# Optimization experiments

Measured on AMD Instinct MI355X. Metric: run time of the kernel, lower is better.

The kernel has to match this reference:

```python
import jax, jax.numpy as jnp
import numpy as np

P = 2; NH = 16; HS = 1024; NL = 12; NC = 1000
B, D, H, W = 32, 64, 32, 32
LFEAT = P * P * D  # 256 per-patch feature dim


def _sincos_1d(dim, pos):
    omega = np.arange(dim // 2, dtype=np.float64) / (dim / 2.0)
    omega = 1.0 / 10000 ** omega
    out = np.einsum('m,d->md', pos.reshape(-1), omega)
    return np.concatenate([np.sin(out), np.cos(out)], axis=1)


def _pos_embed(dim, grid_size):
    g = np.arange(grid_size, dtype=np.float32)
    grid = np.stack(np.meshgrid(g, g), axis=0).reshape(2, 1, grid_size, grid_size)
    emb = np.concatenate([_sincos_1d(dim // 2, grid[0]), _sincos_1d(dim // 2, grid[1])], axis=1)
    return jnp.asarray(emb, dtype=jnp.float32)


def setup_inputs() -> dict:
    key = jax.random.key(0)
    ks = iter(jax.random.split(key, 40))
    def w(shape, s=0.02):
        return jax.random.normal(next(ks), shape, jnp.float32) * s
    return {
        'x': jax.random.normal(next(ks), (B, D, H, W), jnp.float32),
        'y': jax.random.randint(next(ks), (B,), 0, NC),
        't': jax.random.randint(next(ks), (B,), 0, 1000),
        'proj_w': w((LFEAT, HS)), 'proj_b': jnp.zeros((HS,), jnp.float32),
        'pos_embed': _pos_embed(HS, H // P),
        'emb_table': w((NC + 1, HS)),
        'blk_mod_w': w((NL, HS, 6 * HS)), 'blk_mod_b': jnp.zeros((NL, 6 * HS), jnp.float32),
        'blk_wq': w((NL, HS, HS)), 'blk_bq': jnp.zeros((NL, HS), jnp.float32),
        'blk_wk': w((NL, HS, HS)), 'blk_bk': jnp.zeros((NL, HS), jnp.float32),
        'blk_wv': w((NL, HS, HS)), 'blk_bv': jnp.zeros((NL, HS), jnp.float32),
        'blk_wo': w((NL, HS, HS)), 'blk_bo': jnp.zeros((NL, HS), jnp.float32),
        'blk_fc1_w': w((NL, HS, 4 * HS)), 'blk_fc1_b': jnp.zeros((NL, 4 * HS), jnp.float32),
        'blk_fc2_w': w((NL, 4 * HS, HS)), 'blk_fc2_b': jnp.zeros((NL, HS), jnp.float32),
        'fin_mod_w': w((HS, 2 * HS)), 'fin_mod_b': jnp.zeros((2 * HS,), jnp.float32),
        'fin_out_w': w((HS, LFEAT)), 'fin_out_b': jnp.zeros((LFEAT,), jnp.float32),
    }


def _ln(z):
    mu = jnp.mean(z, -1, keepdims=True)
    var = jnp.mean((z - mu) ** 2, -1, keepdims=True)
    return (z - mu) * jax.lax.rsqrt(var + 1e-5)


def _forward(x, y, t, proj_w, proj_b, pos_embed, emb_table,
             blk_mod_w, blk_mod_b, blk_wq, blk_bq, blk_wk, blk_bk, blk_wv, blk_bv,
             blk_wo, blk_bo, blk_fc1_w, blk_fc1_b, blk_fc2_w, blk_fc2_b,
             fin_mod_w, fin_mod_b, fin_out_w, fin_out_b):
    Bc, Dc, Hc, Wc = x.shape
    Hp, Wp = Hc // P, Wc // P
    dh = HS // NH
    # patchify_flatten: (B, L, P*P*D)
    tok = x.reshape(Bc, Dc, Hp, P, Wp, P).transpose(0, 2, 4, 3, 5, 1).reshape(Bc, Hp * Wp, P * P * Dc)
    tok = tok @ proj_w + proj_b + pos_embed[None]
    # timestep_embedding: [cos, sin] order per source
    half = HS // 2
    freqs = jnp.exp(-jnp.log(jnp.float32(10000.0)) * jnp.arange(half, dtype=jnp.float32) / half)
    ang = t.astype(jnp.float32)[:, None] * freqs[None]
    c = jnp.concatenate([jnp.cos(ang), jnp.sin(ang)], axis=-1) + emb_table[y]
    c_act = jax.nn.silu(c)  # each block applies silu to c (c is not mutated across blocks)

    def block(xc, p):
        mw, mb, wq, bq, wk, bk, wv, bv, wo, bo, f1w, f1b, f2w, f2b = p
        mod = c_act @ mw + mb
        sh_a, sc_a, g_a, sh_m, sc_m, g_m = jnp.split(mod, 6, axis=1)
        hx = _ln(xc) * (1 + sc_a[:, None]) + sh_a[:, None]
        def heads(z, wz, bz):
            return (z @ wz + bz).reshape(Bc, -1, NH, dh).transpose(0, 2, 1, 3)
        q, k, v = heads(hx, wq, bq), heads(hx, wk, bk), heads(hx, wv, bv)
        logits = jnp.einsum('bhqd,bhkd->bhqk', q, k) / jnp.sqrt(jnp.float32(dh))
        # non-AR mask buffer is all zeros -> no-op
        attn = jax.nn.softmax(logits, axis=-1)
        o = jnp.einsum('bhqk,bhkd->bhqd', attn, v).transpose(0, 2, 1, 3).reshape(Bc, -1, HS)
        xc = xc + g_a[:, None] * (o @ wo + bo)
        hx = _ln(xc) * (1 + sc_m[:, None]) + sh_m[:, None]
        mlp = jax.nn.gelu(hx @ f1w + f1b, approximate=False) @ f2w + f2b
        return xc + g_m[:, None] * mlp, None

    tok, _ = jax.lax.scan(block, tok, (blk_mod_w, blk_mod_b, blk_wq, blk_bq, blk_wk, blk_bk,
                                       blk_wv, blk_bv, blk_wo, blk_bo,
                                       blk_fc1_w, blk_fc1_b, blk_fc2_w, blk_fc2_b))
    fmod = c_act @ fin_mod_w + fin_mod_b
    sh, sc = jnp.split(fmod, 2, axis=1)
    out = (_ln(tok) * (1 + sc[:, None]) + sh[:, None]) @ fin_out_w + fin_out_b
    # unpatchify -> (B, D, H, W)
    return out.reshape(Bc, Hp, Wp, P, P, Dc).transpose(0, 5, 1, 3, 2, 4).reshape(Bc, Dc, Hc, Wc)


def reference(x, y, t, proj_w, proj_b, pos_embed, emb_table,
              blk_mod_w, blk_mod_b, blk_wq, blk_bq, blk_wk, blk_bk, blk_wv, blk_bv,
              blk_wo, blk_bo, blk_fc1_w, blk_fc1_b, blk_fc2_w, blk_fc2_b,
              fin_mod_w, fin_mod_b, fin_out_w, fin_out_b):
    return _forward(x, y, t, proj_w, proj_b, pos_embed, emb_table,
                    blk_mod_w, blk_mod_b, blk_wq, blk_bq, blk_wk, blk_bk, blk_wv, blk_bv,
                    blk_wo, blk_bo, blk_fc1_w, blk_fc1_b, blk_fc2_w, blk_fc2_b,
                    fin_mod_w, fin_mod_b, fin_out_w, fin_out_b)
```

## Files before the change

kernel.cpp:

```cpp
#include <hip/hip_runtime.h>
#include <hip/hip_bf16.h>
#include <math.h>

typedef short s16x8 __attribute__((ext_vector_type(8)));
typedef float f32x4 __attribute__((ext_vector_type(4)));
typedef unsigned short u16;

#define BAR() __builtin_amdgcn_s_barrier()
#define PRIO1() __builtin_amdgcn_s_setprio(1)
#define PRIO0() __builtin_amdgcn_s_setprio(0)
#define VMCNT0() asm volatile("s_waitcnt vmcnt(0)" ::: "memory")

__device__ __forceinline__ u16 f2b(float f) {
    unsigned u = __builtin_bit_cast(unsigned, f);
    u += 0x7fffu + ((u >> 16) & 1u);
    return (u16)(u >> 16);
}
__device__ __forceinline__ f32x4 mfma16(s16x8 a, s16x8 b, f32x4 c) {
    return __builtin_amdgcn_mfma_f32_16x16x32_bf16(a, b, c, 0, 0, 0);
}
__device__ __forceinline__ void gload16(const void* g, void* l) {
    __builtin_amdgcn_global_load_lds((const __attribute__((address_space(1))) unsigned*)g,
                                     (__attribute__((address_space(3))) unsigned*)l, 16, 0, 0);
}

__global__ __launch_bounds__(256) void patchify_kernel(const float* __restrict__ x, u16* __restrict__ out) {
    int idx = blockIdx.x * 256 + threadIdx.x;
    int row = idx >> 8, col = idx & 255;
    int b = row >> 8, ll = row & 255, hp = ll >> 4, wp = ll & 15;
    int pp = col >> 6, d = col & 63;
    out[idx] = f2b(x[(size_t)((b * 64 + d) * 32 + hp * 2 + (pp >> 1)) * 32 + wp * 2 + (pp & 1)]);
}

__global__ __launch_bounds__(256) void cact_kernel(const int* __restrict__ t, const int* __restrict__ y,
                                                   const float* __restrict__ emb, float* __restrict__ cactF) {
    int b = blockIdx.x, tid = threadIdx.x;
    float tv = (float)t[b];
    int yb = y[b];
#pragma unroll
    for (int j = 0; j < 4; ++j) {
        int c = tid * 4 + j;
        int f = (c < 512) ? c : c - 512;
        float freq = __expf(-9.210340371976184f * (float)f * (1.f / 512.f));
        float ang = tv * freq;
        float v = (c < 512) ? cosf(ang) : sinf(ang);
        v += emb[(size_t)yb * 1024 + c];
        v = v / (1.f + __expf(-v));
        cactF[b * 1024 + c] = v;
    }
}

__global__ __launch_bounds__(256) void bcat_kernel(const float* __restrict__ bq, const float* __restrict__ bk,
                                                   const float* __restrict__ bv, float* __restrict__ out) {
    int lyr = blockIdx.x, j = blockIdx.y, tid = threadIdx.x;
    const float* src = (j == 0) ? bq : ((j == 1) ? bk : bv);
    float4 v = ((const float4*)(src + (size_t)lyr * 1024))[tid];
    ((float4*)(out + (size_t)lyr * 3072 + j * 1024))[tid] = v;
}

__global__ __launch_bounds__(256) void mod32_kernel(const float* __restrict__ cactF, const float* __restrict__ W,
                                                    const float* __restrict__ bias, float* __restrict__ out, int N) {
    __shared__ float cs[32 * 256];
    __shared__ float red[4 * 32 * 64];
    int tid = threadIdx.x, lane = tid & 63, kg = tid >> 6;
    int n = blockIdx.x * 64 + lane;
    float acc[32];
#pragma unroll
    for (int r = 0; r < 32; ++r) acc[r] = 0.f;
    for (int ch = 0; ch < 4; ++ch) {
        __syncthreads();
#pragma unroll
        for (int j = 0; j < 8; ++j) {
            int idx = tid * 4 + j * 1024;
            float4 v = *(const float4*)&cactF[(size_t)(idx >> 8) * 1024 + ch * 256 + (idx & 255)];
            *(float4*)&cs[idx] = v;
        }
        __syncthreads();
        const float* Wp = W + (size_t)(ch * 256 + kg * 64) * N + n;
        for (int kk = 0; kk < 64; kk += 4) {
            float w0 = Wp[(size_t)(kk + 0) * N];
            float w1 = Wp[(size_t)(kk + 1) * N];
            float w2 = Wp[(size_t)(kk + 2) * N];
            float w3 = Wp[(size_t)(kk + 3) * N];
            int kb = kg * 64 + kk;
#pragma unroll
            for (int r = 0; r < 32; ++r) {
                float4 cv = *(const float4*)&cs[r * 256 + kb];
                acc[r] += cv.x * w0 + cv.y * w1 + cv.z * w2 + cv.w * w3;
            }
        }
    }
#pragma unroll
    for (int r = 0; r < 32; ++r) red[(kg * 32 + r) * 64 + lane] = acc[r];
    __syncthreads();
    int r = tid >> 3, j0 = (tid & 7) * 8;
#pragma unroll
    for (int jj = 0; jj < 8; ++jj) {
        int nn = j0 + jj;
        float s = red[(0 * 32 + r) * 64 + nn] + red[(1 * 32 + r) * 64 + nn] +
                  red[(2 * 32 + r) * 64 + nn] + red[(3 * 32 + r) * 64 + nn];
        out[(size_t)r * N + blockIdx.x * 64 + nn] = s + bias[blockIdx.x * 64 + nn];
    }
}

__device__ __forceinline__ void tpose_body(float (*tile)[65], const float* __restrict__ in,
                                           u16* __restrict__ out, int R, int C, int r0, int c0, int tid) {
    int rr = tid >> 4, cc = (tid & 15) * 4;
#pragma unroll
    for (int j = 0; j < 4; ++j) {
        float4 v = *(const float4*)&in[(size_t)(r0 + j * 16 + rr) * C + c0 + cc];
        tile[j * 16 + rr][cc]     = v.x;
        tile[j * 16 + rr][cc + 1] = v.y;
        tile[j * 16 + rr][cc + 2] = v.z;
        tile[j * 16 + rr][cc + 3] = v.w;
    }
    __syncthreads();
    int oc = tid >> 3, r8 = (tid & 7) * 8;
#pragma unroll
    for (int j = 0; j < 2; ++j) {
        int ocl = j * 32 + oc;
        s16x8 vv;
#pragma unroll
        for (int e = 0; e < 8; ++e) vv[e] = (short)f2b(tile[r8 + e][ocl]);
        *(s16x8*)&out[(size_t)(c0 + ocl) * R + r0 + r8] = vv;
    }
}

__global__ __launch_bounds__(256) void transpose_cvt64k(const float* __restrict__ in, u16* __restrict__ out,
                                                        int R, int C) {
    __shared__ float tile[64][65];
    tpose_body(tile, in, out, R, C, blockIdx.y * 64, blockIdx.x * 64, threadIdx.x);
}

__global__ __launch_bounds__(256) void transpose_layer(
    const float* __restrict__ wq, const float* __restrict__ wk,
    const float* __restrict__ wv, const float* __restrict__ wo, const float* __restrict__ f1,
    const float* __restrict__ f2,
    u16* __restrict__ qkvT, u16* __restrict__ woT, u16* __restrict__ f1T, u16* __restrict__ f2T) {
    __shared__ float tile[64][65];
    int bid = blockIdx.x, tid = threadIdx.x;
    const float* src; u16* dst; int R, C, tloc;
    if (bid < 256)       { src = wq; dst = qkvT;               R = 1024; C = 1024; tloc = bid; }
    else if (bid < 512)  { src = wk; dst = qkvT + 1024 * 1024; R = 1024; C = 1024; tloc = bid - 256; }
    else if (bid < 768)  { src = wv; dst = qkvT + 2048 * 1024; R = 1024; C = 1024; tloc = bid - 512; }
    else if (bid < 1024) { src = wo; dst = woT;                R = 1024; C = 1024; tloc = bid - 768; }
    else if (bid < 2048) { src = f1; dst = f1T;                R = 1024; C = 4096; tloc = bid - 1024; }
    else                 { src = f2; dst = f2T;                R = 4096; C = 1024; tloc = bid - 2048; }
    int tx = C >> 6;
    int ty = tloc / tx, txi = tloc - ty * tx;
    tpose_body(tile, src, dst, R, C, ty * 64, txi * 64, tid);
}

__global__ __launch_bounds__(256) void ln_mod_kernel(const float* __restrict__ x, const float* __restrict__ modv,
                                                     int mod_ld, int sh_off, int sc_off, u16* __restrict__ out) {
    int row = blockIdx.x, tid = threadIdx.x, b = row >> 8;
    float4 xv = ((const float4*)(x + (size_t)row * 1024))[tid];
    float s = xv.x + xv.y + xv.z + xv.w;
    float s2 = xv.x * xv.x + xv.y * xv.y + xv.z * xv.z + xv.w * xv.w;
#pragma unroll
    for (int d = 1; d < 64; d <<= 1) { s += __shfl_xor(s, d); s2 += __shfl_xor(s2, d); }
    __shared__ float red[8];
    int w = tid >> 6;
    if ((tid & 63) == 0) { red[w] = s; red[4 + w] = s2; }
    __syncthreads();
    s = red[0] + red[1] + red[2] + red[3];
    s2 = red[4] + red[5] + red[6] + red[7];
    float mu = s * (1.f / 1024.f);
    float rs = rsqrtf(s2 * (1.f / 1024.f) - mu * mu + 1e-5f);
    const float* shp = modv + (size_t)b * mod_ld + sh_off;
    const float* scp = modv + (size_t)b * mod_ld + sc_off;
    float4 sh4 = ((const float4*)shp)[tid];
    float4 sc4 = ((const float4*)scp)[tid];
    u16 o0 = f2b((xv.x - mu) * rs * (1.f + sc4.x) + sh4.x);
    u16 o1 = f2b((xv.y - mu) * rs * (1.f + sc4.y) + sh4.y);
    u16 o2 = f2b((xv.z - mu) * rs * (1.f + sc4.z) + sh4.z);
    u16 o3 = f2b((xv.w - mu) * rs * (1.f + sc4.w) + sh4.w);
    unsigned long long pk = (unsigned long long)o0 | ((unsigned long long)o1 << 16) |
                            ((unsigned long long)o2 << 32) | ((unsigned long long)o3 << 48);
    *(unsigned long long*)&out[(size_t)row * 1024 + tid * 4] = pk;
}

template <int EPI>
__global__ __launch_bounds__(512, 1) void gemm8(
    const u16* __restrict__ A, int lda, const u16* __restrict__ Bt, int ldb,
    int M, int N, int K, const float* __restrict__ bias,
    float* __restrict__ outF, u16* __restrict__ outB, int ldc,
    const float* __restrict__ aux1, const float* __restrict__ aux2, int gateOff) {
    __shared__ u16 As[3][256 * 64];
    __shared__ u16 Bs[3][128 * 64];

    const int tid = threadIdx.x, w = tid >> 6, l = tid & 63;
    const int wm = w >> 1, wn = w & 1;

    const int nbn = N >> 7;
    const int orig = blockIdx.x;
    const int cpx = gridDim.x >> 3;
    const int wg = (orig & 7) * cpx + (orig >> 3);
    const int bm = wg / nbn, bn = wg - bm * nbn;
    const int row0 = bm << 8, col0 = bn << 7;

    const int NT = K >> 6;

    const int srow = tid >> 3, sslot = tid & 7;
    const int ksl = sslot ^ (srow & 7);
    const u16* gA = A + (size_t)(row0 + srow) * lda + ksl * 8;
    const u16* gB = Bt + (size_t)(col0 + srow) * ldb + ksl * 8;
    const int lOff = srow * 64 + sslot * 8;

    const int fr = l & 15, fg = l >> 4;
    const int arow = wm * 64 + fr;
    const int brow = wn * 64 + fr;

    f32x4 acc[4][4];
#pragma unroll
    for (int m = 0; m < 4; ++m)
#pragma unroll
        for (int n = 0; n < 4; ++n) acc[m][n] = (f32x4){0.f, 0.f, 0.f, 0.f};

    {
        u16* a0 = &As[0][lOff];
        u16* b0 = &Bs[0][lOff];
#pragma unroll
        for (int a = 0; a < 4; ++a) gload16(gA + (size_t)a * 64 * lda, a0 + a * 4096);
#pragma unroll
        for (int b = 0; b < 2; ++b) gload16(gB + (size_t)b * 64 * ldb, b0 + b * 4096);
        if (NT > 1) {
            u16* a1 = &As[1][lOff];
#pragma unroll
            for (int a = 0; a < 3; ++a) gload16(gA + (size_t)a * 64 * lda + 64, a1 + a * 4096);
        }
    }
    if (NT > 1) { asm volatile("s_waitcnt vmcnt(3)" ::: "memory"); }
    else        { VMCNT0(); }
    BAR();
    __builtin_amdgcn_sched_barrier(0);

    int q = 0;
    for (int t = 0; t < NT; ++t) {
        const u16* ca = As[q];
        const u16* cb = Bs[q];
        const int q1 = (q == 2) ? 0 : q + 1;
        const int q2 = (q1 == 2) ? 0 : q1 + 1;

        s16x8 af[4][2], bf[4][2];
#pragma unroll
        for (int m = 0; m < 4; ++m) {
            int r = arow + m * 16;
            af[m][0] = *(const s16x8*)(ca + r * 64 + ((fg     ^ (r & 7)) * 8));
            af[m][1] = *(const s16x8*)(ca + r * 64 + (((4 + fg) ^ (r & 7)) * 8));
        }
#pragma unroll
        for (int n = 0; n < 2; ++n) {
            int r = brow + n * 16;
            bf[n][0] = *(const s16x8*)(cb + r * 64 + ((fg     ^ (r & 7)) * 8));
            bf[n][1] = *(const s16x8*)(cb + r * 64 + (((4 + fg) ^ (r & 7)) * 8));
        }
        if (t + 1 < NT) {
            gload16(gA + (size_t)(3 * 64) * lda + (size_t)(t + 1) * 64, &As[q1][lOff] + 3 * 4096);
            gload16(gB + (size_t)(t + 1) * 64, &Bs[q1][lOff]);
            gload16(gB + (size_t)(1 * 64) * ldb + (size_t)(t + 1) * 64, &Bs[q1][lOff] + 4096);
        }
        BAR(); PRIO1();
#pragma unroll
        for (int m = 0; m < 4; ++m)
#pragma unroll
            for (int n = 0; n < 2; ++n) {
                acc[m][n] = mfma16(af[m][0], bf[n][0], acc[m][n]);
                acc[m][n] = mfma16(af[m][1], bf[n][1], acc[m][n]);
            }
        PRIO0(); BAR();
#pragma unroll
        for (int n = 0; n < 2; ++n) {
            int r = brow + (n + 2) * 16;
            bf[n + 2][0] = *(const s16x8*)(cb + r * 64 + ((fg     ^ (r & 7)) * 8));
            bf[n + 2][1] = *(const s16x8*)(cb + r * 64 + (((4 + fg) ^ (r & 7)) * 8));
        }
        if (t + 2 < NT) {
#pragma unroll
            for (int a = 0; a < 3; ++a)
                gload16(gA + (size_t)a * 64 * lda + (size_t)(t + 2) * 64, &As[q2][lOff] + a * 4096);
        }
        BAR(); PRIO1();
#pragma unroll
        for (int m = 0; m < 4; ++m)
#pragma unroll
            for (int n = 2; n < 4; ++n) {
                acc[m][n] = mfma16(af[m][0], bf[n][0], acc[m][n]);
                acc[m][n] = mfma16(af[m][1], bf[n][1], acc[m][n]);
            }
        PRIO0();
        if (t < NT - 2)       { asm volatile("s_waitcnt vmcnt(3)" ::: "memory"); }
        else if (t == NT - 2) { VMCNT0(); }
        if (t < NT - 1) {
            BAR();
            __builtin_amdgcn_sched_barrier(0);
        }
        q = q1;
    }

    const int erow = row0 + wm * 64 + fg * 4;
    const int ecol = col0 + wn * 64 + fr;
#pragma unroll
    for (int m = 0; m < 4; ++m) {
#pragma unroll
        for (int n = 0; n < 4; ++n) {
#pragma unroll
            for (int r = 0; r < 4; ++r) {
                int row = erow + m * 16 + r;
                int col = ecol + n * 16;
                float v = acc[m][n][r];
                if constexpr (EPI == 1) {
                    outB[(size_t)row * ldc + col] = f2b(v + bias[col]);
                } else if constexpr (EPI == 2) {
                    outF[(size_t)row * ldc + col] = v + bias[col] + aux1[(size_t)(row & 255) * 1024 + col];
                } else if constexpr (EPI == 3) {
                    outF[(size_t)row * ldc + col] =
                        aux1[(size_t)row * ldc + col] +
                        aux2[(size_t)(row >> 8) * 6144 + gateOff + col] * (v + bias[col]);
                } else {
                    float xg = v + bias[col];
                    outB[(size_t)row * ldc + col] = f2b(0.5f * xg * (1.f + erff(xg * 0.70710678118654752f)));
                }
            }
        }
    }
}

__global__ __launch_bounds__(256, 2) void gemm_fin(
    const u16* __restrict__ A, int lda, const u16* __restrict__ Bt, int ldb,
    int M, int N, int K, const float* __restrict__ bias, float* outF) {
    __shared__ u16 Asl[128 * 32];
    __shared__ u16 Bsl[128 * 32];
    const int tid = threadIdx.x, w = tid >> 6, l = tid & 63;
    const int row0 = blockIdx.y * 128, col0 = blockIdx.x * 128;
    const int wm = w >> 1, wn = w & 1;

    f32x4 acc[4][4];
#pragma unroll
    for (int m = 0; m < 4; ++m)
#pragma unroll
        for (int n = 0; n < 4; ++n) acc[m][n] = (f32x4){0.f, 0.f, 0.f, 0.f};

    const int rA0 = w * 16 + (l >> 2), rA1 = rA0 + 64;
    const int kc = (l & 3) * 8;
    const u16* a0 = A + (size_t)(row0 + rA0) * lda + kc;
    const u16* a1 = A + (size_t)(row0 + rA1) * lda + kc;
    const u16* b0 = Bt + (size_t)(col0 + rA0) * ldb + kc;
    const u16* b1 = Bt + (size_t)(col0 + rA1) * ldb + kc;
    u16* la0 = &Asl[rA0 * 32 + kc];
    u16* la1 = &Asl[rA1 * 32 + kc];
    u16* lb0 = &Bsl[rA0 * 32 + kc];
    u16* lb1 = &Bsl[rA1 * 32 + kc];

    for (int k0 = 0; k0 < K; k0 += 32) {
        __syncthreads();
        gload16(a0 + k0, la0);
        gload16(a1 + k0, la1);
        gload16(b0 + k0, lb0);
        gload16(b1 + k0, lb1);
        __syncthreads();
        s16x8 af[4], bfr[4];
#pragma unroll
        for (int m = 0; m < 4; ++m)
            af[m] = *(const s16x8*)&Asl[(wm * 64 + m * 16 + (l & 15)) * 32 + (l >> 4) * 8];
#pragma unroll
        for (int n = 0; n < 4; ++n)
            bfr[n] = *(const s16x8*)&Bsl[(wn * 64 + n * 16 + (l & 15)) * 32 + (l >> 4) * 8];
#pragma unroll
        for (int m = 0; m < 4; ++m)
#pragma unroll
            for (int n = 0; n < 4; ++n) acc[m][n] = mfma16(af[m], bfr[n], acc[m][n]);
    }

#pragma unroll
    for (int m = 0; m < 4; ++m) {
#pragma unroll
        for (int n = 0; n < 4; ++n) {
#pragma unroll
            for (int r = 0; r < 4; ++r) {
                int row = row0 + wm * 64 + m * 16 + (l >> 4) * 4 + r;
                int col = col0 + wn * 64 + n * 16 + (l & 15);
                float xg = acc[m][n][r] + bias[col];
                int bb = row >> 8, ll = row & 255, hp = ll >> 4, wp = ll & 15;
                int pp = col >> 6, d = col & 63;
                outF[(size_t)((bb * 64 + d) * 32 + hp * 2 + (pp >> 1)) * 32 + wp * 2 + (pp & 1)] = xg;
            }
        }
    }
}

__global__ __launch_bounds__(256, 2) void attn_kernel(const u16* __restrict__ qkv, u16* __restrict__ obuf) {
    __shared__ u16 Qs[64 * 64];
    __shared__ u16 Ks[256 * 64];
    __shared__ u16 VTs[64 * 256];
    int qt = blockIdx.x, h = blockIdx.y, b = blockIdx.z;
    int tid = threadIdx.x, w = tid >> 6, l = tid & 63;
    size_t base = (size_t)b * 256 * 3072;

    {
        int r = tid >> 2;
#pragma unroll
        for (int j = 0; j < 2; ++j) {
            int sg = (tid & 3) + j * 4;
            *(s16x8*)&Qs[r * 64 + sg * 8] =
                *(const s16x8*)&qkv[base + (size_t)(qt * 64 + r) * 3072 + h * 64 + sg * 8];
        }
    }
#pragma unroll
    for (int j = 0; j < 8; ++j) {
        int i = tid + j * 256;
        int r = i >> 3, sg = i & 7;
        *(s16x8*)&Ks[r * 64 + sg * 8] =
            *(const s16x8*)&qkv[base + (size_t)r * 3072 + 1024 + h * 64 + sg * 8];
    }
#pragma unroll
    for (int j = 0; j < 8; ++j) {
        int i = tid + j * 256;
        int r = i >> 3, sg = i & 7;
        s16x8 v = *(const s16x8*)&qkv[base + (size_t)r * 3072 + 2048 + h * 64 + sg * 8];
#pragma unroll
        for (int e = 0; e < 8; ++e) VTs[(sg * 8 + e) * 256 + r] = ((const u16*)&v)[e];
    }
    __syncthreads();

    s16x8 aq0 = *(const s16x8*)&Qs[(w * 16 + (l & 15)) * 64 + (l >> 4) * 8];
    s16x8 aq1 = *(const s16x8*)&Qs[(w * 16 + (l & 15)) * 64 + 32 + (l >> 4) * 8];
    f32x4 sf[16];
#pragma unroll
    for (int cf = 0; cf < 16; ++cf) {
        f32x4 a = (f32x4){0.f, 0.f, 0.f, 0.f};
        s16x8 bk0 = *(const s16x8*)&Ks[(cf * 16 + (l & 15)) * 64 + (l >> 4) * 8];
        s16x8 bk1 = *(const s16x8*)&Ks[(cf * 16 + (l & 15)) * 64 + 32 + (l >> 4) * 8];
        a = mfma16(aq0, bk0, a);
        a = mfma16(aq1, bk1, a);
        sf[cf] = a * 0.125f;
    }
    __syncthreads();

#pragma unroll
    for (int r = 0; r < 4; ++r) {
        float m = -1e30f;
#pragma unroll
        for (int cf = 0; cf < 16; ++cf) m = fmaxf(m, sf[cf][r]);
#pragma unroll
        for (int d = 1; d < 16; d <<= 1) m = fmaxf(m, __shfl_xor(m, d));
        float sm = 0.f;
#pragma unroll
        for (int cf = 0; cf < 16; ++cf) { float e = __expf(sf[cf][r] - m); sf[cf][r] = e; sm += e; }
#pragma unroll
        for (int d = 1; d < 16; d <<= 1) sm += __shfl_xor(sm, d);
        float inv = 1.f / sm;
        int rl = w * 16 + (l >> 4) * 4 + r;
#pragma unroll
        for (int cf = 0; cf < 16; ++cf) Ks[rl * 256 + cf * 16 + (l & 15)] = f2b(sf[cf][r] * inv);
    }
    __syncthreads();

    f32x4 oacc[4];
#pragma unroll
    for (int cf = 0; cf < 4; ++cf) oacc[cf] = (f32x4){0.f, 0.f, 0.f, 0.f};
#pragma unroll
    for (int ks = 0; ks < 8; ++ks) {
        s16x8 ap = *(const s16x8*)&Ks[(w * 16 + (l & 15)) * 256 + ks * 32 + (l >> 4) * 8];
#pragma unroll
        for (int cf = 0; cf < 4; ++cf) {
            s16x8 bv = *(const s16x8*)&VTs[(cf * 16 + (l & 15)) * 256 + ks * 32 + (l >> 4) * 8];
            oacc[cf] = mfma16(ap, bv, oacc[cf]);
        }
    }
    size_t orow0 = (size_t)(b * 256 + qt * 64 + w * 16);
#pragma unroll
    for (int cf = 0; cf < 4; ++cf)
#pragma unroll
        for (int r = 0; r < 4; ++r) {
            int rr = (l >> 4) * 4 + r;
            obuf[(orow0 + rr) * 1024 + h * 64 + cf * 16 + (l & 15)] = f2b(oacc[cf][r]);
        }
}

extern "C" void kernel_launch(void* const* d_in, const int* in_sizes, int n_in,
                              void* d_out, int out_size, void* d_ws, size_t ws_size,
                              hipStream_t stream) {
    (void)in_sizes; (void)n_in; (void)out_size; (void)ws_size;
    const float* x         = (const float*)d_in[0];
    const int*   y         = (const int*)d_in[1];
    const int*   t         = (const int*)d_in[2];
    const float* proj_w    = (const float*)d_in[3];
    const float* proj_b    = (const float*)d_in[4];
    const float* pos_embed = (const float*)d_in[5];
    const float* emb_table = (const float*)d_in[6];
    const float* blk_mod_w = (const float*)d_in[7];
    const float* blk_mod_b = (const float*)d_in[8];
    const float* blk_wq    = (const float*)d_in[9];
    const float* blk_bq    = (const float*)d_in[10];
    const float* blk_wk    = (const float*)d_in[11];
    const float* blk_bk    = (const float*)d_in[12];
    const float* blk_wv    = (const float*)d_in[13];
    const float* blk_bv    = (const float*)d_in[14];
    const float* blk_wo    = (const float*)d_in[15];
    const float* blk_bo    = (const float*)d_in[16];
    const float* blk_f1w   = (const float*)d_in[17];
    const float* blk_f1b   = (const float*)d_in[18];
    const float* blk_f2w   = (const float*)d_in[19];
    const float* blk_f2b   = (const float*)d_in[20];
    const float* fin_mod_w = (const float*)d_in[21];
    const float* fin_mod_b = (const float*)d_in[22];
    const float* fin_out_w = (const float*)d_in[23];
    const float* fin_out_b = (const float*)d_in[24];
    float* out = (float*)d_out;

    char* ws = (char*)d_ws;
    size_t off = 0;
    auto alloc = [&](size_t bytes) -> char* {
        char* p = ws + off;
        off += (bytes + 255) & ~(size_t)255;
        return p;
    };
    float* xc    = (float*)alloc(8192ull * 1024 * 4);
    u16*   hx    = (u16*)alloc(8192ull * 1024 * 2);
    u16*   qkvb  = (u16*)alloc(8192ull * 3072 * 2);
    u16*   obufp = (u16*)alloc(8192ull * 1024 * 2);
    u16*   h1    = (u16*)alloc(8192ull * 4096 * 2);
    u16*   patchA= (u16*)alloc(8192ull * 256 * 2);
    float* cactF = (float*)alloc(32ull * 1024 * 4);
    float* modb  = (float*)alloc(32ull * 6144 * 4);
    float* fmod  = (float*)alloc(32ull * 2048 * 4);
    float* bqkv  = (float*)alloc(12ull * 3072 * 4);
    u16*   projT = (u16*)alloc(1024ull * 256 * 2);
    u16*   foT   = (u16*)alloc(256ull * 1024 * 2);
    u16*   qkvT  = (u16*)alloc(3072ull * 1024 * 2);
    u16*   woT   = (u16*)alloc(1024ull * 1024 * 2);
    u16*   f1T   = (u16*)alloc(4096ull * 1024 * 2);
    u16*   f2T   = (u16*)alloc(1024ull * 4096 * 2);

    patchify_kernel<<<8192, 256, 0, stream>>>(x, patchA);
    cact_kernel<<<32, 256, 0, stream>>>(t, y, emb_table, cactF);
    bcat_kernel<<<dim3(12, 3), 256, 0, stream>>>(blk_bq, blk_bk, blk_bv, bqkv);
    transpose_cvt64k<<<dim3(16, 4), 256, 0, stream>>>(proj_w, projT, 256, 1024);
    transpose_cvt64k<<<dim3(4, 16), 256, 0, stream>>>(fin_out_w, foT, 1024, 256);
    mod32_kernel<<<32, 256, 0, stream>>>(cactF, fin_mod_w, fin_mod_b, fmod, 2048);

    gemm8<2><<<256, 512, 0, stream>>>(patchA, 256, projT, 256, 8192, 1024, 256,
                                      proj_b, xc, nullptr, 1024, pos_embed, nullptr, 0);

    for (int i = 0; i < 12; ++i) {
        transpose_layer<<<3072, 256, 0, stream>>>(
            blk_wq + (size_t)i * 1024 * 1024, blk_wk + (size_t)i * 1024 * 1024,
            blk_wv + (size_t)i * 1024 * 1024, blk_wo + (size_t)i * 1024 * 1024,
            blk_f1w + (size_t)i * 1024 * 4096, blk_f2w + (size_t)i * 4096 * 1024,
            qkvT, woT, f1T, f2T);

        mod32_kernel<<<96, 256, 0, stream>>>(cactF, blk_mod_w + (size_t)i * 1024 * 6144,
                                             blk_mod_b + (size_t)i * 6144, modb, 6144);
        ln_mod_kernel<<<8192, 256, 0, stream>>>(xc, modb, 6144, 0, 1024, hx);
        gemm8<1><<<768, 512, 0, stream>>>(hx, 1024, qkvT, 1024, 8192, 3072, 1024,
                                          bqkv + (size_t)i * 3072, nullptr, qkvb, 3072,
                                          nullptr, nullptr, 0);
        attn_kernel<<<dim3(4, 16, 32), 256, 0, stream>>>(qkvb, obufp);
        gemm8<3><<<256, 512, 0, stream>>>(obufp, 1024, woT, 1024, 8192, 1024, 1024,
                                          blk_bo + (size_t)i * 1024, xc, nullptr, 1024,
                                          xc, modb, 2048);
        ln_mod_kernel<<<8192, 256, 0, stream>>>(xc, modb, 6144, 3072, 4096, hx);
        gemm8<4><<<1024, 512, 0, stream>>>(hx, 1024, f1T, 1024, 8192, 4096, 1024,
                                           blk_f1b + (size_t)i * 4096, nullptr, h1, 4096,
                                           nullptr, nullptr, 0);
        gemm8<3><<<256, 512, 0, stream>>>(h1, 4096, f2T, 4096, 8192, 1024, 4096,
                                          blk_f2b + (size_t)i * 1024, xc, nullptr, 1024,
                                          xc, modb, 5120);
    }
    ln_mod_kernel<<<8192, 256, 0, stream>>>(xc, fmod, 2048, 0, 1024, hx);
    gemm_fin<<<dim3(2, 64), 256, 0, stream>>>(hx, 1024, foT, 1024, 8192, 256, 1024,
                                              fin_out_b, out);
}
```

Measured before the change: 5.576 ms.

## Add 256x256-tile pipelined GEMM for QKV and FC1 projections

After: 6.422 ms. +15.2%, slower.

```diff
diff --git a/kernel.cpp b/kernel.cpp
--- a/kernel.cpp
+++ b/kernel.cpp
@@ -9,6 +9,7 @@
 #define BAR() __builtin_amdgcn_s_barrier()
 #define PRIO1() __builtin_amdgcn_s_setprio(1)
 #define PRIO0() __builtin_amdgcn_s_setprio(0)
+#define VMCNT4() asm volatile("s_waitcnt vmcnt(4)" ::: "memory")
 #define VMCNT0() asm volatile("s_waitcnt vmcnt(0)" ::: "memory")
 
 __device__ __forceinline__ u16 f2b(float f) {
@@ -181,6 +182,137 @@
 }
 
 template <int EPI>
+__global__ __launch_bounds__(512, 2) void gemm256q(
+    const u16* __restrict__ A, int lda, const u16* __restrict__ Bt, int ldb,
+    int M, int N, int K, const float* __restrict__ bias, u16* __restrict__ outB, int ldc) {
+    __shared__ u16 Aq[2][2][2][4096];
+    __shared__ u16 Bq[2][2][2][4096];
+
+    const int tid = threadIdx.x, w = tid >> 6, l = tid & 63;
+    const int wm = w >> 2, wn = w & 3;
+    const int fr = l & 15, fg = l >> 4;
+
+    const int nbn = N >> 8;
+    const int cpx = gridDim.x >> 3;
+    const int wg = (blockIdx.x & 7) * cpx + (blockIdx.x >> 3);
+    const int bm = wg / nbn, bn = wg - bm * nbn;
+    const int row0 = bm << 8, col0 = bn << 8;
+    const int NT = K >> 6;
+
+    const int srow = tid >> 2;
+    const int sgq  = tid & 3;
+    const int sx   = sgq ^ (srow & 3) ^ ((srow >> 2) & 3);
+    const int sdst = tid * 8;
+
+    auto stA = [&](int d, int kkh, int t) {
+#pragma unroll
+        for (int h = 0; h < 2; ++h) {
+            const u16* src = A + (size_t)(row0 + h * 128 + srow) * lda + (size_t)t * 64 + (kkh * 4 + sx) * 8;
+            gload16(src, &Aq[d][h][kkh][sdst]);
+        }
+    };
+    auto stB = [&](int d, int kkh, int t) {
+#pragma unroll
+        for (int h = 0; h < 2; ++h) {
+            const u16* src = Bt + (size_t)(col0 + h * 128 + srow) * ldb + (size_t)t * 64 + (kkh * 4 + sx) * 8;
+            gload16(src, &Bq[d][h][kkh][sdst]);
+        }
+    };
+
+    const int slotc = (fg ^ (fr & 3) ^ ((fr >> 2) & 3)) * 8;
+    auto LDA = [&](int d, int mh, int kkh, s16x8 (&out)[4]) {
+#pragma unroll
+        for (int m = 0; m < 4; ++m) {
+            int r = mh * 64 + m * 16 + fr;
+            out[m] = *(const s16x8*)&Aq[d][wm][kkh][r * 32 + slotc];
+        }
+    };
+    auto LDB = [&](int d, int kkh, s16x8 (&out)[4]) {
+#pragma unroll
+        for (int n = 0; n < 4; ++n) {
+            int r = (wn & 1) * 64 + n * 16 + fr;
+            out[n] = *(const s16x8*)&Bq[d][wn >> 1][kkh][r * 32 + slotc];
+        }
+    };
+
+    f32x4 acc[8][4];
+#pragma unroll
+    for (int m = 0; m < 8; ++m)
+#pragma unroll
+        for (int n = 0; n < 4; ++n) acc[m][n] = (f32x4){0.f, 0.f, 0.f, 0.f};
+
+    auto MQ = [&](int mh, s16x8 (&Af)[4], s16x8 (&Bf)[4]) {
+#pragma unroll
+        for (int m = 0; m < 4; ++m)
+#pragma unroll
+            for (int n = 0; n < 4; ++n)
+                acc[mh * 4 + m][n] = mfma16(Af[m], Bf[n], acc[mh * 4 + m][n]);
+    };
+
+    stA(0, 0, 0); stB(0, 0, 0); stA(0, 1, 0); stB(0, 1, 0);
+    if (NT > 1) { stA(1, 0, 1); stB(1, 0, 1); VMCNT4(); }
+    else        { VMCNT0(); }
+    BAR();
+    __builtin_amdgcn_sched_barrier(0);
+
+    const int iters = NT >> 1;
+    for (int j = 0; j < iters; ++j) {
+        const int T1 = 2 * j + 1, Tn0 = 2 * j + 2, Tn1 = 2 * j + 3;
+        const bool more = Tn0 < NT;
+        s16x8 Af[4], Bf[4];
+        LDA(0, 0, 0, Af); LDB(0, 0, Bf);
+        stA(1, 1, T1);
+        BAR(); PRIO1(); MQ(0, Af, Bf); PRIO0(); BAR();
+        LDA(0, 1, 0, Af);
+        stB(1, 1, T1);
+        BAR(); PRIO1(); MQ(1, Af, Bf); PRIO0(); BAR();
+        LDA(0, 0, 1, Af); LDB(0, 1, Bf);
+        if (more) stA(0, 0, Tn0);
+        BAR(); PRIO1(); MQ(0, Af, Bf); PRIO0(); BAR();
+        LDA(0, 1, 1, Af);
+        if (more) stB(0, 0, Tn0);
+        BAR(); PRIO1(); MQ(1, Af, Bf); PRIO0();
+        if (more) { VMCNT4(); } else { VMCNT0(); }
+        BAR();
+        LDA(1, 0, 0, Af); LDB(1, 0, Bf);
+        if (more) stA(0, 1, Tn0);
+        BAR(); PRIO1(); MQ(0, Af, Bf); PRIO0(); BAR();
+        LDA(1, 1, 0, Af);
+        if (more) stB(0, 1, Tn0);
+        BAR(); PRIO1(); MQ(1, Af, Bf); PRIO0(); BAR();
+        LDA(1, 0, 1, Af); LDB(1, 1, Bf);
+        if (more) stA(1, 0, Tn1);
+        BAR(); PRIO1(); MQ(0, Af, Bf); PRIO0(); BAR();
+        LDA(1, 1, 1, Af);
+        if (more) stB(1, 0, Tn1);
+        BAR(); PRIO1(); MQ(1, Af, Bf); PRIO0();
+        if (more) {
+            VMCNT4();
+            BAR();
+            __builtin_amdgcn_sched_barrier(0);
+        }
+    }
+
+#pragma unroll
+    for (int mi = 0; mi < 8; ++mi) {
+#pragma unroll
+        for (int n = 0; n < 4; ++n) {
+#pragma unroll
+            for (int r = 0; r < 4; ++r) {
+                int row = row0 + wm * 128 + mi * 16 + fg * 4 + r;
+                int col = col0 + wn * 64 + n * 16 + fr;
+                float v = acc[mi][n][r] + bias[col];
+                if constexpr (EPI == 1) {
+                    outB[(size_t)row * ldc + col] = f2b(v);
+                } else {
+                    outB[(size_t)row * ldc + col] = f2b(0.5f * v * (1.f + erff(v * 0.70710678118654752f)));
+                }
+            }
+        }
+    }
+}
+
+template <int EPI>
 __global__ __launch_bounds__(512, 1) void gemm8(
     const u16* __restrict__ A, int lda, const u16* __restrict__ Bt, int ldb,
     int M, int N, int K, const float* __restrict__ bias,
@@ -309,17 +441,12 @@
                 int row = erow + m * 16 + r;
                 int col = ecol + n * 16;
                 float v = acc[m][n][r];
-                if constexpr (EPI == 1) {
-                    outB[(size_t)row * ldc + col] = f2b(v + bias[col]);
-                } else if constexpr (EPI == 2) {
+                if constexpr (EPI == 2) {
                     outF[(size_t)row * ldc + col] = v + bias[col] + aux1[(size_t)(row & 255) * 1024 + col];
-                } else if constexpr (EPI == 3) {
+                } else {
                     outF[(size_t)row * ldc + col] =
                         aux1[(size_t)row * ldc + col] +
                         aux2[(size_t)(row >> 8) * 6144 + gateOff + col] * (v + bias[col]);
-                } else {
-                    float xg = v + bias[col];
-                    outB[(size_t)row * ldc + col] = f2b(0.5f * xg * (1.f + erff(xg * 0.70710678118654752f)));
                 }
             }
         }
@@ -553,17 +680,15 @@
         mod32_kernel<<<96, 256, 0, stream>>>(cactF, blk_mod_w + (size_t)i * 1024 * 6144,
                                              blk_mod_b + (size_t)i * 6144, modb, 6144);
         ln_mod_kernel<<<8192, 256, 0, stream>>>(xc, modb, 6144, 0, 1024, hx);
-        gemm8<1><<<768, 512, 0, stream>>>(hx, 1024, qkvT, 1024, 8192, 3072, 1024,
-                                          bqkv + (size_t)i * 3072, nullptr, qkvb, 3072,
-                                          nullptr, nullptr, 0);
+        gemm256q<1><<<384, 512, 0, stream>>>(hx, 1024, qkvT, 1024, 8192, 3072, 1024,
+                                             bqkv + (size_t)i * 3072, qkvb, 3072);
         attn_kernel<<<dim3(4, 16, 32), 256, 0, stream>>>(qkvb, obufp);
         gemm8<3><<<256, 512, 0, stream>>>(obufp, 1024, woT, 1024, 8192, 1024, 1024,
                                           blk_bo + (size_t)i * 1024, xc, nullptr, 1024,
                                           xc, modb, 2048);
         ln_mod_kernel<<<8192, 256, 0, stream>>>(xc, modb, 6144, 3072, 4096, hx);
-        gemm8<4><<<1024, 512, 0, stream>>>(hx, 1024, f1T, 1024, 8192, 4096, 1024,
-                                           blk_f1b + (size_t)i * 4096, nullptr, h1, 4096,
-                                           nullptr, nullptr, 0);
+        gemm256q<4><<<512, 512, 0, stream>>>(hx, 1024, f1T, 1024, 8192, 4096, 1024,
+                                             blk_f1b + (size_t)i * 4096, h1, 4096);
         gemm8<3><<<256, 512, 0, stream>>>(h1, 4096, f2T, 4096, 8192, 1024, 4096,
                                           blk_f2b + (size_t)i * 1024, xc, nullptr, 1024,
                                           xc, modb, 5120);
```
